# Kernel optimization log

Hardware: AMD Instinct MI355X
Metric: run time of the kernel (lower is better)

## Reference

```python
import jax, jax.numpy as jnp
import numpy as np
import math

B, L, H, NH = 8, 200, 128, 2
HD = H // NH  # head dim = 64
TIME_VOCAB = 32
LN_EPS = 1e-12


def setup_inputs() -> dict:
    key = jax.random.key(0)
    ks = jax.random.split(key, 16)
    rn = lambda k, shape, s=0.02: (jax.random.normal(k, shape, jnp.float32) * s)
    return {
        "input_tensor": jax.random.normal(ks[0], (B, L, H), jnp.float32),
        "time_seq": jnp.sort(jax.random.randint(ks[1], (B, L), 0, 100000, jnp.int64), axis=-1),
        "attention_mask": jnp.zeros((B, 1, L, L), jnp.float32),
        "Wq": rn(ks[2], (H, H)), "bq": jnp.zeros((H,), jnp.float32),
        "Wk": rn(ks[3], (H, H)), "bk": jnp.zeros((H,), jnp.float32),
        "Wv": rn(ks[4], (H, H)), "bv": jnp.zeros((H,), jnp.float32),
        "Wd": rn(ks[5], (H, H)), "bd": jnp.zeros((H,), jnp.float32),
        "ln_g": jnp.ones((H,), jnp.float32), "ln_b": jnp.zeros((H,), jnp.float32),
        "key_time_table": rn(ks[6], (TIME_VOCAB, H)),
        "value_time_table": rn(ks[7], (TIME_VOCAB, H)),
        "key_pos_table": rn(ks[8], (L, H)),
        "value_pos_table": rn(ks[9], (L, H)),
    }


def _split_heads(x):
    # [B, L, H] -> [B, NH, L, HD]
    b, l, _ = x.shape
    return x.reshape(b, l, NH, HD).transpose(0, 2, 1, 3)


def reference(input_tensor, time_seq, attention_mask,
              Wq, bq, Wk, bk, Wv, bv, Wd, bd, ln_g, ln_b,
              key_time_table, value_time_table, key_pos_table, value_pos_table):
    b, l, h = input_tensor.shape

    # position embeddings (same for all batches)
    kpos = key_pos_table[:l].reshape(l, NH, HD).transpose(1, 0, 2)[None]    # [1,NH,L,HD]
    vpos = value_pos_table[:l].reshape(l, NH, HD).transpose(1, 0, 2)[None]  # [1,NH,L,HD]

    q = _split_heads(input_tensor @ Wq + bq)  # [B,NH,L,HD]
    k = _split_heads(input_tensor @ Wk + bk)
    v = _split_heads(input_tensor @ Wv + bv)

    scores = jnp.einsum('bhqd,bhkd->bhqk', q, k + kpos)

    # time decay: diff[b,i,j] = floor(log(1 + |t_i - t_j|))
    t = time_seq
    diff_idx = jnp.log1p(jnp.abs(t[:, :, None] - t[:, None, :]).astype(jnp.float32)).astype(jnp.int32)  # [B,L,L]

    # [B,L,L,H] -> [B,NH,L,L,HD]
    kt = key_time_table[diff_idx].reshape(b, l, l, NH, HD).transpose(0, 3, 1, 2, 4)
    vt = value_time_table[diff_idx].reshape(b, l, l, NH, HD).transpose(0, 3, 1, 2, 4)

    time_scores = jnp.einsum('bhqd,bhqkd->bhqk', q, kt)

    scores = (scores + time_scores) / math.sqrt(HD)
    scores = scores + attention_mask  # additive mask, broadcast over heads

    probs = jax.nn.softmax(scores, axis=-1)  # attn_dropout is identity in eval

    ctx = jnp.einsum('bhqk,bhkd->bhqd', probs, v + vpos)
    # NOTE: original uses raw (masked, pre-softmax) attention_scores here
    time_ctx = jnp.einsum('bhqk,bhqkd->bhqd', scores, vt)
    ctx = ctx + time_ctx

    ctx = ctx.transpose(0, 2, 1, 3).reshape(b, l, h)  # merge heads
    hidden = ctx @ Wd + bd                            # out_dropout identity in eval

    x = hidden + input_tensor
    mu = x.mean(-1, keepdims=True)
    var = ((x - mu) ** 2).mean(-1, keepdims=True)
    return (x - mu) / jnp.sqrt(var + LN_EPS) * ln_g + ln_b
```

## Files before the change

kernel.cpp:

```cpp
#include <hip/hip_runtime.h>
#include <math.h>

#define B_ 8
#define L_ 200
#define H_ 128
#define NH_ 2
#define HD_ 64
#define LP_ 256
#define TV_ 32
#define RQ_ 8
#define TQ_ 4

__global__ __launch_bounds__(128)
void qkv_kernel(const float* __restrict__ X,
                const float* __restrict__ Wq, const float* __restrict__ bq,
                const float* __restrict__ Wk, const float* __restrict__ bk,
                const float* __restrict__ Wv, const float* __restrict__ bv,
                const float* __restrict__ kpt, const float* __restrict__ vpt,
                float* __restrict__ Q, float* __restrict__ Kt, float* __restrict__ Vp){
    const int r0 = blockIdx.x * RQ_;
    const int m  = blockIdx.y;
    const int j  = threadIdx.x;
    __shared__ float xs[RQ_][H_];
    #pragma unroll
    for (int r = 0; r < RQ_; ++r) xs[r][j] = X[(r0 + r) * H_ + j];
    __syncthreads();
    const float* W = (m == 0) ? Wq : ((m == 1) ? Wk : Wv);
    float acc[RQ_];
    #pragma unroll
    for (int r = 0; r < RQ_; ++r) acc[r] = 0.f;
    #pragma unroll 4
    for (int i = 0; i < H_; ++i) {
        const float w = W[i * H_ + j];
        #pragma unroll
        for (int r = 0; r < RQ_; ++r) acc[r] += xs[r][i] * w;
    }
    const int h = j >> 6, d = j & 63;
    if (m == 0) {
        const float bj = bq[j];
        #pragma unroll
        for (int r = 0; r < RQ_; ++r) Q[(r0 + r) * H_ + j] = acc[r] + bj;
    } else if (m == 1) {
        const float bj = bk[j];
        #pragma unroll
        for (int r = 0; r < RQ_; ++r) {
            const int row = r0 + r, b = row / L_, l = row % L_;
            Kt[((b * NH_ + h) * HD_ + d) * LP_ + l] = acc[r] + bj + kpt[l * H_ + j];
        }
    } else {
        const float bj = bv[j];
        #pragma unroll
        for (int r = 0; r < RQ_; ++r) {
            const int row = r0 + r, b = row / L_, l = row % L_;
            Vp[((b * NH_ + h) * L_ + l) * HD_ + d] = acc[r] + bj + vpt[l * H_ + j];
        }
    }
}

__global__ __launch_bounds__(512)
void attn_out_kernel(const float* __restrict__ Q, const float* __restrict__ Kt,
                     const float* __restrict__ Vp, const int* __restrict__ tseq,
                     const float* __restrict__ mask,
                     const float* __restrict__ ktt, const float* __restrict__ vtt,
                     const float* __restrict__ Wd, const float* __restrict__ bd,
                     const float* __restrict__ X, const float* __restrict__ g,
                     const float* __restrict__ bb, float* __restrict__ out){
    const int b  = blockIdx.x / (L_ / TQ_);
    const int q0 = (blockIdx.x % (L_ / TQ_)) * TQ_;
    const int w  = threadIdx.x >> 6, lane = threadIdx.x & 63;
    const int h  = w & 1, qr = w >> 1, q = q0 + qr;
    const int bh = b * NH_ + h;

    __shared__ __align__(16) float qs [8][HD_];
    __shared__ float qkt[8][TV_];
    __shared__ float ss [8][TV_];
    __shared__ __align__(16) float ps [8][LP_];
    __shared__ float ctx_s[TQ_][H_];
    __shared__ float red1[8], red2[8];

    qs[w][lane] = Q[(b * L_ + q) * H_ + h * HD_ + lane];
    if (lane < TV_) ss[w][lane] = 0.f;
    if (lane < TV_) {
        float a = 0.f;
        #pragma unroll 8
        for (int d = 0; d < HD_; ++d) a += qs[w][d] * ktt[lane * H_ + h * HD_ + d];
        qkt[w][lane] = a;
    }

    const float4* kt4 = (const float4*)(Kt + (size_t)bh * HD_ * LP_);
    float4 s4 = make_float4(0.f, 0.f, 0.f, 0.f);
    #pragma unroll 4
    for (int d = 0; d < HD_; ++d) {
        const float qd = qs[w][d];
        const float4 kv = kt4[d * (LP_ / 4) + lane];
        s4.x += qd * kv.x; s4.y += qd * kv.y; s4.z += qd * kv.z; s4.w += qd * kv.w;
    }
    float sv[4] = {s4.x, s4.y, s4.z, s4.w};
    const int k0 = lane * 4;
    float mx = -INFINITY;
    if (k0 < L_) {
        const float4 m4 = ((const float4*)(mask + ((size_t)(b * L_ + q)) * L_))[lane];
        const int4   t4 = ((const int4*)(tseq + b * L_))[lane];
        const int    tq = tseq[b * L_ + q];
        const float mv[4] = {m4.x, m4.y, m4.z, m4.w};
        const int   tk[4] = {t4.x, t4.y, t4.z, t4.w};
        #pragma unroll
        for (int jj = 0; jj < 4; ++jj) {
            int dt = tq - tk[jj]; if (dt < 0) dt = -dt;
            int idx = (int)log1pf((float)dt);
            if (idx > TV_ - 1) idx = TV_ - 1;
            float s = (sv[jj] + qkt[w][idx]) * 0.125f + mv[jj];
            sv[jj] = s;
            atomicAdd(&ss[w][idx], s);
            if (s > mx) mx = s;
        }
    } else {
        sv[0] = sv[1] = sv[2] = sv[3] = -INFINITY;
    }
    for (int off = 32; off; off >>= 1) { float o = __shfl_xor(mx, off); if (o > mx) mx = o; }
    float sum = 0.f, ev[4];
    #pragma unroll
    for (int jj = 0; jj < 4; ++jj) {
        float e = (k0 + jj < L_) ? __expf(sv[jj] - mx) : 0.f;
        ev[jj] = e; sum += e;
    }
    for (int off = 32; off; off >>= 1) sum += __shfl_xor(sum, off);
    ((float4*)ps[w])[lane] = make_float4(ev[0], ev[1], ev[2], ev[3]);

    const float inv = 1.f / sum;
    const float* vp = Vp + (size_t)bh * L_ * HD_;
    float c = 0.f;
    #pragma unroll 4
    for (int k = 0; k < L_; ++k) c += ps[w][k] * vp[k * HD_ + lane];
    c *= inv;
    float tc = 0.f;
    #pragma unroll 8
    for (int i = 0; i < TV_; ++i) tc += ss[w][i] * vtt[i * H_ + h * HD_ + lane];
    ctx_s[qr][h * HD_ + lane] = c + tc;
    __syncthreads();

    const int r = threadIdx.x >> 7, j = threadIdx.x & 127;
    float acc = 0.f;
    #pragma unroll 8
    for (int i = 0; i < H_; ++i) acc += ctx_s[r][i] * Wd[i * H_ + j];
    const int row = b * L_ + q0 + r;
    const float x = acc + bd[j] + X[row * H_ + j];

    float s = x;
    for (int off = 32; off; off >>= 1) s += __shfl_xor(s, off);
    if (lane == 0) red1[w] = s;
    __syncthreads();
    const float mean = (red1[2 * r] + red1[2 * r + 1]) * (1.f / H_);
    const float dx = x - mean;
    float s2 = dx * dx;
    for (int off = 32; off; off >>= 1) s2 += __shfl_xor(s2, off);
    if (lane == 0) red2[w] = s2;
    __syncthreads();
    const float var = (red2[2 * r] + red2[2 * r + 1]) * (1.f / H_);
    const float y = dx * rsqrtf(var + 1e-12f) * g[j] + bb[j];
    out[row * H_ + j] = y;
}

extern "C" void kernel_launch(void* const* d_in, const int* in_sizes, int n_in,
                              void* d_out, int out_size, void* d_ws, size_t ws_size,
                              hipStream_t stream) {
    const float* X    = (const float*)d_in[0];
    const int*   tseq = (const int*)  d_in[1];
    const float* mask = (const float*)d_in[2];
    const float* Wq = (const float*)d_in[3],  *bq = (const float*)d_in[4];
    const float* Wk = (const float*)d_in[5],  *bk = (const float*)d_in[6];
    const float* Wv = (const float*)d_in[7],  *bv = (const float*)d_in[8];
    const float* Wd = (const float*)d_in[9],  *bd = (const float*)d_in[10];
    const float* g  = (const float*)d_in[11], *bb = (const float*)d_in[12];
    const float* ktt = (const float*)d_in[13], *vtt = (const float*)d_in[14];
    const float* kpt = (const float*)d_in[15], *vpt = (const float*)d_in[16];

    float* ws  = (float*)d_ws;
    float* Q   = ws;
    float* Kt  = Q   + B_ * L_ * H_;
    float* Vp  = Kt  + B_ * NH_ * HD_ * LP_;

    dim3 g1(B_ * L_ / RQ_, 3);
    qkv_kernel<<<g1, 128, 0, stream>>>(X, Wq, bq, Wk, bk, Wv, bv, kpt, vpt, Q, Kt, Vp);
    attn_out_kernel<<<B_ * (L_ / TQ_), 512, 0, stream>>>(Q, Kt, Vp, tseq, mask, ktt, vtt,
                                                         Wd, bd, X, g, bb, (float*)d_out);
}
```

Measured before the change: 140.7 us.

## Halve queries per attention block and stage time tables in shared memory

Each attention block now handles 2 query rows with 256 threads instead of 4 with 512, doubling the grid. The key and value time tables are copied into padded shared memory per block. The query·time-table dot products are spread over the full wave with a shuffle reduction, and the score loop uses two accumulators. A few unroll factors are also raised. The aim is more blocks for latency hiding and no more strided global reads of the time tables, but every block now pays for a 32 KB table copy and a larger LDS footprint that may limit occupancy.

New measurement: 121.2 us. -13.8%, faster.

```diff
diff --git a/kernel.cpp b/kernel.cpp
--- a/kernel.cpp
+++ b/kernel.cpp
@@ -9,7 +9,7 @@
 #define LP_ 256
 #define TV_ 32
 #define RQ_ 8
-#define TQ_ 4
+#define TQ_ 2
 
 __global__ __launch_bounds__(128)
 void qkv_kernel(const float* __restrict__ X,
@@ -29,7 +29,7 @@
     float acc[RQ_];
     #pragma unroll
     for (int r = 0; r < RQ_; ++r) acc[r] = 0.f;
-    #pragma unroll 4
+    #pragma unroll 8
     for (int i = 0; i < H_; ++i) {
         const float w = W[i * H_ + j];
         #pragma unroll
@@ -57,7 +57,7 @@
     }
 }
 
-__global__ __launch_bounds__(512)
+__global__ __launch_bounds__(256)
 void attn_out_kernel(const float* __restrict__ Q, const float* __restrict__ Kt,
                      const float* __restrict__ Vp, const int* __restrict__ tseq,
                      const float* __restrict__ mask,
@@ -71,34 +71,48 @@
     const int h  = w & 1, qr = w >> 1, q = q0 + qr;
     const int bh = b * NH_ + h;
 
-    __shared__ __align__(16) float qs [8][HD_];
-    __shared__ float qkt[8][TV_];
-    __shared__ float ss [8][TV_];
-    __shared__ __align__(16) float ps [8][LP_];
+    __shared__ float ktt_s[TV_][H_ + 1];
+    __shared__ float vtt_s[TV_][H_ + 1];
+    __shared__ __align__(16) float qs [4][HD_];
+    __shared__ float qkt[4][TV_];
+    __shared__ float ss [4][TV_];
+    __shared__ __align__(16) float ps [4][LP_];
     __shared__ float ctx_s[TQ_][H_];
-    __shared__ float red1[8], red2[8];
-
+    __shared__ float red1[4], red2[4];
+
+    for (int t = threadIdx.x; t < TV_ * H_; t += 256) {
+        ktt_s[t >> 7][t & 127] = ktt[t];
+        vtt_s[t >> 7][t & 127] = vtt[t];
+    }
     qs[w][lane] = Q[(b * L_ + q) * H_ + h * HD_ + lane];
     if (lane < TV_) ss[w][lane] = 0.f;
-    if (lane < TV_) {
+    __syncthreads();
+
+    {
+        const int i = lane & 31, half = lane >> 5;
         float a = 0.f;
         #pragma unroll 8
-        for (int d = 0; d < HD_; ++d) a += qs[w][d] * ktt[lane * H_ + h * HD_ + d];
-        qkt[w][lane] = a;
+        for (int d = 0; d < 32; ++d)
+            a += qs[w][half * 32 + d] * ktt_s[i][h * HD_ + half * 32 + d];
+        a += __shfl_xor(a, 32);
+        if (lane < TV_) qkt[w][lane] = a;
     }
 
     const float4* kt4 = (const float4*)(Kt + (size_t)bh * HD_ * LP_);
-    float4 s4 = make_float4(0.f, 0.f, 0.f, 0.f);
-    #pragma unroll 4
-    for (int d = 0; d < HD_; ++d) {
-        const float qd = qs[w][d];
-        const float4 kv = kt4[d * (LP_ / 4) + lane];
-        s4.x += qd * kv.x; s4.y += qd * kv.y; s4.z += qd * kv.z; s4.w += qd * kv.w;
-    }
-    float sv[4] = {s4.x, s4.y, s4.z, s4.w};
-    const int k0 = lane * 4;
+    float4 sA = make_float4(0.f, 0.f, 0.f, 0.f);
+    float4 sB = make_float4(0.f, 0.f, 0.f, 0.f);
+    #pragma unroll 8
+    for (int d = 0; d < HD_; d += 2) {
+        const float q0d = qs[w][d], q1d = qs[w][d + 1];
+        const float4 k0 = kt4[d * (LP_ / 4) + lane];
+        const float4 k1 = kt4[(d + 1) * (LP_ / 4) + lane];
+        sA.x += q0d * k0.x; sA.y += q0d * k0.y; sA.z += q0d * k0.z; sA.w += q0d * k0.w;
+        sB.x += q1d * k1.x; sB.y += q1d * k1.y; sB.z += q1d * k1.z; sB.w += q1d * k1.w;
+    }
+    float sv[4] = {sA.x + sB.x, sA.y + sB.y, sA.z + sB.z, sA.w + sB.w};
+    const int k0i = lane * 4;
     float mx = -INFINITY;
-    if (k0 < L_) {
+    if (k0i < L_) {
         const float4 m4 = ((const float4*)(mask + ((size_t)(b * L_ + q)) * L_))[lane];
         const int4   t4 = ((const int4*)(tseq + b * L_))[lane];
         const int    tq = tseq[b * L_ + q];
@@ -121,7 +135,7 @@
     float sum = 0.f, ev[4];
     #pragma unroll
     for (int jj = 0; jj < 4; ++jj) {
-        float e = (k0 + jj < L_) ? __expf(sv[jj] - mx) : 0.f;
+        float e = (k0i + jj < L_) ? __expf(sv[jj] - mx) : 0.f;
         ev[jj] = e; sum += e;
     }
     for (int off = 32; off; off >>= 1) sum += __shfl_xor(sum, off);
@@ -130,12 +144,12 @@
     const float inv = 1.f / sum;
     const float* vp = Vp + (size_t)bh * L_ * HD_;
     float c = 0.f;
-    #pragma unroll 4
+    #pragma unroll 8
     for (int k = 0; k < L_; ++k) c += ps[w][k] * vp[k * HD_ + lane];
     c *= inv;
     float tc = 0.f;
     #pragma unroll 8
-    for (int i = 0; i < TV_; ++i) tc += ss[w][i] * vtt[i * H_ + h * HD_ + lane];
+    for (int i = 0; i < TV_; ++i) tc += ss[w][i] * vtt_s[i][h * HD_ + lane];
     ctx_s[qr][h * HD_ + lane] = c + tc;
     __syncthreads();
 
@@ -182,6 +196,6 @@
 
     dim3 g1(B_ * L_ / RQ_, 3);
     qkv_kernel<<<g1, 128, 0, stream>>>(X, Wq, bq, Wk, bk, Wv, bv, kpt, vpt, Q, Kt, Vp);
-    attn_out_kernel<<<B_ * (L_ / TQ_), 512, 0, stream>>>(Q, Kt, Vp, tseq, mask, ktt, vtt,
+    attn_out_kernel<<<B_ * (L_ / TQ_), 256, 0, stream>>>(Q, Kt, Vp, tseq, mask, ktt, vtt,
                                                          Wd, bd, X, g, bb, (float*)d_out);
 }
```
